# Optimization experiments

Measured on AMD Instinct MI355X. Metric: run time of the kernel, lower is better.

The kernel has to match this reference:

```python
import jax, jax.numpy as jnp
import numpy as np

N_NODES = 1_000_000
N_EDGES = 16_000_000
BATCH = 1_000_000
EMBED_DIM = 3


def setup_inputs() -> dict:
    key = jax.random.key(0)
    ks = jax.random.split(key, 11)
    edge_index = jax.random.randint(ks[0], (2, N_EDGES), 0, N_NODES, dtype=jnp.int32)
    edge_weight = jax.random.uniform(ks[1], (N_EDGES,), dtype=jnp.float32) + 0.1
    home = jax.random.randint(ks[2], (BATCH,), 0, N_NODES, dtype=jnp.int32)
    away = jax.random.randint(ks[3], (BATCH,), 0, N_NODES, dtype=jnp.int32)
    emb = jax.random.normal(ks[4], (N_NODES, EMBED_DIM), dtype=jnp.float32)
    w_conv = jax.random.normal(ks[5], (3, 3), dtype=jnp.float32) * 0.5
    b_conv = jax.random.normal(ks[6], (3,), dtype=jnp.float32) * 0.1
    w1 = jax.random.normal(ks[7], (6, 6), dtype=jnp.float32) * 0.4
    b1 = jax.random.normal(ks[8], (6,), dtype=jnp.float32) * 0.1
    w3 = jax.random.normal(ks[9], (6, 3), dtype=jnp.float32) * 0.4
    b3 = jax.random.normal(ks[10], (3,), dtype=jnp.float32) * 0.1
    return {"edge_index": edge_index, "edge_weight": edge_weight, "home": home,
            "away": away, "emb": emb, "w_conv": w_conv, "b_conv": b_conv,
            "w1": w1, "b1": b1, "w3": w3, "b3": b3}


def reference(edge_index, edge_weight, home, away, emb, w_conv, b_conv, w1, b1, w3, b3):
    n = emb.shape[0]
    row, col = edge_index[0], edge_index[1]
    # gcn_norm (symmetric, add_self_loops=False): deg over target nodes
    deg = jax.ops.segment_sum(edge_weight, col, num_segments=n)
    dinv = jnp.where(deg > 0, jax.lax.rsqrt(jnp.where(deg > 0, deg, 1.0)), 0.0)
    norm = dinv[row] * edge_weight * dinv[col]  # [E]
    x = emb @ w_conv                            # [N,3] transformed features
    msg = norm[:, None] * x[row]                # [E,3] gather + scale
    agg = jax.ops.segment_sum(msg, col, num_segments=n) + b_conv  # [N,3]
    x = jax.nn.leaky_relu(agg)                  # conv1 output
    h = jnp.concatenate([x[home], x[away]], axis=-1)  # [B,6]
    h = jax.nn.leaky_relu(h @ w1 + b1)          # lin1
    h = jax.nn.leaky_relu(h @ w3 + b3)          # lin3 -> [B,3]
    return jax.nn.log_softmax(h, axis=0)        # LogSoftmax over dim=0 as in source
```

## Files before the change

### kernel.cpp

```cpp
#include <hip/hip_runtime.h>
#include <hip/hip_fp16.h>
#include <math.h>

#define NN 1000000
#define NE 16000000
#define NB 1000000
#define NEQ (NE / 4)
#define BN 4096
#define NBUCK 245
#define NBUCKR 256
#define NBLK 1024
#define SSPLIT 4
#define CMASK 0xFFFFFu

__device__ __forceinline__ float leaky(float v) { return v > 0.f ? v : 0.01f * v; }

__device__ __forceinline__ uint2 pack_h4(float x, float y, float z) {
    __half2 a = __floats2half2_rn(x, y);
    __half2 b = __floats2half2_rn(z, 0.f);
    uint2 u;
    u.x = *(unsigned int*)&a;
    u.y = *(unsigned int*)&b;
    return u;
}

__device__ __forceinline__ float3 unpack_h4(uint2 u) {
    __half2 a = *(__half2*)&u.x;
    __half2 b = *(__half2*)&u.y;
    float2 fa = __half22float2(a);
    return make_float3(fa.x, fa.y, __low2float(b));
}

__device__ __forceinline__ void atomicMaxF(float* addr, float val) {
    unsigned int* ia = (unsigned int*)addr;
    unsigned int old = *ia;
    while (true) {
        float f = __uint_as_float(old);
        if (f >= val) break;
        unsigned int prev = atomicCAS(ia, old, __float_as_uint(val));
        if (prev == old) break;
        old = prev;
    }
}

__global__ void init_stats(float* stats) {
    int t = threadIdx.x;
    if (t < 3) stats[t] = -1e30f;
    else if (t < 6) stats[t] = 0.f;
}

__global__ __launch_bounds__(256) void count_kernel(const int4* __restrict__ col4,
                                                    unsigned int* __restrict__ HG) {
    __shared__ unsigned int h[NBUCKR];
    h[threadIdx.x] = 0u;
    __syncthreads();
    int stride = gridDim.x * 256;
    for (int i = blockIdx.x * 256 + threadIdx.x; i < NEQ; i += stride) {
        int4 c = col4[i];
        atomicAdd(&h[((unsigned int)c.x) >> 12], 1u);
        atomicAdd(&h[((unsigned int)c.y) >> 12], 1u);
        atomicAdd(&h[((unsigned int)c.z) >> 12], 1u);
        atomicAdd(&h[((unsigned int)c.w) >> 12], 1u);
    }
    __syncthreads();
    HG[(size_t)threadIdx.x * NBLK + blockIdx.x] = h[threadIdx.x];
}

__global__ __launch_bounds__(256) void scan_sum(const unsigned int* __restrict__ HG,
                                                unsigned int* __restrict__ part) {
    const unsigned int* p = HG + (size_t)blockIdx.x * NBLK;
    unsigned int s = 0;
    for (int i = threadIdx.x; i < NBLK; i += 256) s += p[i];
    #pragma unroll
    for (int off = 32; off > 0; off >>= 1) s += __shfl_down(s, off);
    __shared__ unsigned int sm[4];
    int wave = threadIdx.x >> 6, lane = threadIdx.x & 63;
    if (lane == 0) sm[wave] = s;
    __syncthreads();
    if (threadIdx.x == 0) part[blockIdx.x] = sm[0] + sm[1] + sm[2] + sm[3];
}

__global__ void scan_part(unsigned int* part) {
    __shared__ unsigned int tmp[256];
    int t = threadIdx.x;
    unsigned int v = part[t];
    tmp[t] = v;
    __syncthreads();
    for (int off = 1; off < 256; off <<= 1) {
        unsigned int add = (t >= off) ? tmp[t - off] : 0u;
        __syncthreads();
        tmp[t] += add;
        __syncthreads();
    }
    part[t] = tmp[t] - v;
}

__global__ __launch_bounds__(256) void scan_apply(unsigned int* __restrict__ HG,
                                                  const unsigned int* __restrict__ part) {
    __shared__ unsigned int vals[NBLK];
    __shared__ unsigned int ts[256];
    int t = threadIdx.x;
    unsigned int* p = HG + (size_t)blockIdx.x * NBLK;
    for (int i = t; i < NBLK; i += 256) vals[i] = p[i];
    __syncthreads();
    unsigned int a0 = vals[4 * t], a1 = vals[4 * t + 1], a2 = vals[4 * t + 2], a3 = vals[4 * t + 3];
    unsigned int ls = a0 + a1 + a2 + a3;
    ts[t] = ls;
    __syncthreads();
    for (int off = 1; off < 256; off <<= 1) {
        unsigned int add = (t >= off) ? ts[t - off] : 0u;
        __syncthreads();
        ts[t] += add;
        __syncthreads();
    }
    unsigned int base = part[blockIdx.x] + ts[t] - ls;
    p[4 * t] = base;
    p[4 * t + 1] = base + a0;
    p[4 * t + 2] = base + a0 + a1;
    p[4 * t + 3] = base + a0 + a1 + a2;
}

__global__ __launch_bounds__(256) void scatter_kernel(const int4* __restrict__ row4,
                                                      const int4* __restrict__ col4,
                                                      const float4* __restrict__ w4,
                                                      const unsigned int* __restrict__ HG,
                                                      uint2* __restrict__ rec) {
    __shared__ unsigned int pos[NBUCKR];
    pos[threadIdx.x] = HG[(size_t)threadIdx.x * NBLK + blockIdx.x];
    __syncthreads();
    int stride = gridDim.x * 256;
    for (int i = blockIdx.x * 256 + threadIdx.x; i < NEQ; i += stride) {
        int4 r = row4[i];
        int4 c = col4[i];
        float4 w = w4[i];
        {
            unsigned int cu = (unsigned int)c.x;
            unsigned int p = atomicAdd(&pos[cu >> 12], 1u);
            rec[p] = make_uint2((unsigned int)r.x | ((cu & 4095u) << 20), __float_as_uint(w.x));
        }
        {
            unsigned int cu = (unsigned int)c.y;
            unsigned int p = atomicAdd(&pos[cu >> 12], 1u);
            rec[p] = make_uint2((unsigned int)r.y | ((cu & 4095u) << 20), __float_as_uint(w.y));
        }
        {
            unsigned int cu = (unsigned int)c.z;
            unsigned int p = atomicAdd(&pos[cu >> 12], 1u);
            rec[p] = make_uint2((unsigned int)r.z | ((cu & 4095u) << 20), __float_as_uint(w.z));
        }
        {
            unsigned int cu = (unsigned int)c.w;
            unsigned int p = atomicAdd(&pos[cu >> 12], 1u);
            rec[p] = make_uint2((unsigned int)r.w | ((cu & 4095u) << 20), __float_as_uint(w.w));
        }
    }
}

__global__ __launch_bounds__(512) void bucket_deg_kernel(const uint2* __restrict__ rec,
                                                         const unsigned int* __restrict__ HG,
                                                         float* __restrict__ deg_g) {
    __shared__ float degl[BN];
    int b = blockIdx.x % NBUCK;
    int sp = blockIdx.x / NBUCK;
    for (int t = threadIdx.x; t < BN; t += 512) degl[t] = 0.f;
    unsigned int s0 = HG[(size_t)b * NBLK];
    unsigned int e0 = HG[(size_t)(b + 1) * NBLK];
    unsigned int n = e0 - s0;
    unsigned int beg = s0 + (unsigned int)((unsigned long long)n * sp / SSPLIT);
    unsigned int end = s0 + (unsigned int)((unsigned long long)n * (sp + 1) / SSPLIT);
    __syncthreads();
    unsigned int i = beg + threadIdx.x;
    for (; i + 1536 < end; i += 2048) {
        uint2 r0 = rec[i], r1 = rec[i + 512], r2 = rec[i + 1024], r3 = rec[i + 1536];
        atomicAdd(&degl[r0.x >> 20], __uint_as_float(r0.y));
        atomicAdd(&degl[r1.x >> 20], __uint_as_float(r1.y));
        atomicAdd(&degl[r2.x >> 20], __uint_as_float(r2.y));
        atomicAdd(&degl[r3.x >> 20], __uint_as_float(r3.y));
    }
    for (; i < end; i += 512) {
        uint2 r0 = rec[i];
        atomicAdd(&degl[r0.x >> 20], __uint_as_float(r0.y));
    }
    __syncthreads();
    int node0 = b * BN;
    for (int t = threadIdx.x; t < BN; t += 512) {
        float v = degl[t];
        if (v != 0.f) atomicAdd(&deg_g[node0 + t], v);
    }
}

__global__ __launch_bounds__(256) void node1_kernel(const float* __restrict__ deg_g,
                                                    const float* __restrict__ emb,
                                                    const float* __restrict__ w_conv,
                                                    float* __restrict__ dinv,
                                                    uint2* __restrict__ y) {
    int g = blockIdx.x * 256 + threadIdx.x;
    if (g >= NN) return;
    float d = deg_g[g];
    float di = d > 0.f ? rsqrtf(d) : 0.f;
    dinv[g] = di;
    float e0 = emb[3 * g], e1 = emb[3 * g + 1], e2 = emb[3 * g + 2];
    float x0 = e0 * w_conv[0] + e1 * w_conv[3] + e2 * w_conv[6];
    float x1 = e0 * w_conv[1] + e1 * w_conv[4] + e2 * w_conv[7];
    float x2 = e0 * w_conv[2] + e1 * w_conv[5] + e2 * w_conv[8];
    y[g] = pack_h4(di * x0, di * x1, di * x2);
}

__global__ __launch_bounds__(512) void bucket_agg_kernel(const uint2* __restrict__ rec,
                                                         const unsigned int* __restrict__ HG,
                                                         const uint2* __restrict__ y,
                                                         float* __restrict__ acc_g) {
    __shared__ float acc[BN * 3];
    int b = blockIdx.x % NBUCK;
    int sp = blockIdx.x / NBUCK;
    for (int t = threadIdx.x; t < BN * 3; t += 512) acc[t] = 0.f;
    unsigned int s0 = HG[(size_t)b * NBLK];
    unsigned int e0 = HG[(size_t)(b + 1) * NBLK];
    unsigned int n = e0 - s0;
    unsigned int beg = s0 + (unsigned int)((unsigned long long)n * sp / SSPLIT);
    unsigned int end = s0 + (unsigned int)((unsigned long long)n * (sp + 1) / SSPLIT);
    __syncthreads();
    unsigned int i = beg + threadIdx.x;
    for (; i + 1536 < end; i += 2048) {
        uint2 r0 = rec[i], r1 = rec[i + 512], r2 = rec[i + 1024], r3 = rec[i + 1536];
        uint2 u0 = y[r0.x & CMASK];
        uint2 u1 = y[r1.x & CMASK];
        uint2 u2 = y[r2.x & CMASK];
        uint2 u3 = y[r3.x & CMASK];
        float3 y0 = unpack_h4(u0), y1 = unpack_h4(u1), y2 = unpack_h4(u2), y3 = unpack_h4(u3);
        float w0 = __uint_as_float(r0.y), w1 = __uint_as_float(r1.y);
        float w2 = __uint_as_float(r2.y), w3 = __uint_as_float(r3.y);
        unsigned int c0 = (r0.x >> 20) * 3, c1 = (r1.x >> 20) * 3;
        unsigned int c2 = (r2.x >> 20) * 3, c3 = (r3.x >> 20) * 3;
        atomicAdd(&acc[c0 + 0], w0 * y0.x); atomicAdd(&acc[c0 + 1], w0 * y0.y); atomicAdd(&acc[c0 + 2], w0 * y0.z);
        atomicAdd(&acc[c1 + 0], w1 * y1.x); atomicAdd(&acc[c1 + 1], w1 * y1.y); atomicAdd(&acc[c1 + 2], w1 * y1.z);
        atomicAdd(&acc[c2 + 0], w2 * y2.x); atomicAdd(&acc[c2 + 1], w2 * y2.y); atomicAdd(&acc[c2 + 2], w2 * y2.z);
        atomicAdd(&acc[c3 + 0], w3 * y3.x); atomicAdd(&acc[c3 + 1], w3 * y3.y); atomicAdd(&acc[c3 + 2], w3 * y3.z);
    }
    for (; i < end; i += 512) {
        uint2 r0 = rec[i];
        float3 y0 = unpack_h4(y[r0.x & CMASK]);
        float w0 = __uint_as_float(r0.y);
        unsigned int c0 = (r0.x >> 20) * 3;
        atomicAdd(&acc[c0 + 0], w0 * y0.x); atomicAdd(&acc[c0 + 1], w0 * y0.y); atomicAdd(&acc[c0 + 2], w0 * y0.z);
    }
    __syncthreads();
    size_t base = (size_t)b * BN * 3;
    for (int t = threadIdx.x; t < BN * 3; t += 512) {
        float v = acc[t];
        if (v != 0.f) atomicAdd(&acc_g[base + t], v);
    }
}

__global__ __launch_bounds__(256) void node2_kernel(const float* __restrict__ acc_g,
                                                    const float* __restrict__ dinv,
                                                    const float* __restrict__ b_conv,
                                                    uint2* __restrict__ xf) {
    int g = blockIdx.x * 256 + threadIdx.x;
    if (g >= NN) return;
    float di = dinv[g];
    float a0 = acc_g[3 * (size_t)g], a1 = acc_g[3 * (size_t)g + 1], a2 = acc_g[3 * (size_t)g + 2];
    xf[g] = pack_h4(leaky(di * a0 + b_conv[0]),
                    leaky(di * a1 + b_conv[1]),
                    leaky(di * a2 + b_conv[2]));
}

__global__ __launch_bounds__(256) void batch_kernel(const int4* __restrict__ home4,
                                                    const int4* __restrict__ away4,
                                                    const uint2* __restrict__ xf,
                                                    const float* __restrict__ w1,
                                                    const float* __restrict__ b1,
                                                    const float* __restrict__ w3,
                                                    const float* __restrict__ b3,
                                                    float4* __restrict__ out4,
                                                    float* __restrict__ stats, int nq) {
    int i = blockIdx.x * blockDim.x + threadIdx.x;
    float m0 = -1e30f, m1 = -1e30f, m2 = -1e30f;
    if (i < nq) {
        float W1[36], B1[6], W3[18], B3[3];
        #pragma unroll
        for (int k = 0; k < 36; k++) W1[k] = w1[k];
        #pragma unroll
        for (int k = 0; k < 6; k++) B1[k] = b1[k];
        #pragma unroll
        for (int k = 0; k < 18; k++) W3[k] = w3[k];
        #pragma unroll
        for (int k = 0; k < 3; k++) B3[k] = b3[k];

        int4 hh = home4[i], aa = away4[i];
        int hs[4] = {hh.x, hh.y, hh.z, hh.w};
        int as_[4] = {aa.x, aa.y, aa.z, aa.w};
        float o[12];
        #pragma unroll
        for (int e = 0; e < 4; e++) {
            float3 xh = unpack_h4(xf[hs[e]]);
            float3 xa = unpack_h4(xf[as_[e]]);
            float h[6] = {xh.x, xh.y, xh.z, xa.x, xa.y, xa.z};
            float l1v[6];
            #pragma unroll
            for (int j = 0; j < 6; j++) {
                float s = B1[j];
                #pragma unroll
                for (int k = 0; k < 6; k++) s += h[k] * W1[k * 6 + j];
                l1v[j] = leaky(s);
            }
            float o3[3];
            #pragma unroll
            for (int j = 0; j < 3; j++) {
                float s = B3[j];
                #pragma unroll
                for (int k = 0; k < 6; k++) s += l1v[k] * W3[k * 3 + j];
                o3[j] = leaky(s);
            }
            o[3 * e + 0] = o3[0];
            o[3 * e + 1] = o3[1];
            o[3 * e + 2] = o3[2];
            m0 = fmaxf(m0, o3[0]);
            m1 = fmaxf(m1, o3[1]);
            m2 = fmaxf(m2, o3[2]);
        }
        #pragma unroll
        for (int q = 0; q < 3; q++)
            out4[3 * (size_t)i + q] = make_float4(o[4 * q], o[4 * q + 1], o[4 * q + 2], o[4 * q + 3]);
    }
    #pragma unroll
    for (int off = 32; off > 0; off >>= 1) {
        m0 = fmaxf(m0, __shfl_down(m0, off));
        m1 = fmaxf(m1, __shfl_down(m1, off));
        m2 = fmaxf(m2, __shfl_down(m2, off));
    }
    __shared__ float sm[3][4];
    int wave = threadIdx.x >> 6, lane = threadIdx.x & 63;
    if (lane == 0) { sm[0][wave] = m0; sm[1][wave] = m1; sm[2][wave] = m2; }
    __syncthreads();
    if (threadIdx.x == 0) {
        atomicMaxF(&stats[0], fmaxf(fmaxf(sm[0][0], sm[0][1]), fmaxf(sm[0][2], sm[0][3])));
        atomicMaxF(&stats[1], fmaxf(fmaxf(sm[1][0], sm[1][1]), fmaxf(sm[1][2], sm[1][3])));
        atomicMaxF(&stats[2], fmaxf(fmaxf(sm[2][0], sm[2][1]), fmaxf(sm[2][2], sm[2][3])));
    }
}

__global__ __launch_bounds__(256) void sumexp_kernel(const float4* __restrict__ out4,
                                                     float* __restrict__ stats, int nq) {
    float mx0 = stats[0], mx1 = stats[1], mx2 = stats[2];
    int i = blockIdx.x * blockDim.x + threadIdx.x;
    float s0 = 0.f, s1 = 0.f, s2 = 0.f;
    if (i < nq) {
        float4 v = out4[i];
        float vals[4] = {v.x, v.y, v.z, v.w};
        int c = (4 * i) % 3;
        #pragma unroll
        for (int e = 0; e < 4; e++) {
            float mv = (c == 0) ? mx0 : ((c == 1) ? mx1 : mx2);
            float ee = expf(vals[e] - mv);
            if (c == 0) s0 += ee; else if (c == 1) s1 += ee; else s2 += ee;
            c = (c == 2) ? 0 : (c + 1);
        }
    }
    #pragma unroll
    for (int off = 32; off > 0; off >>= 1) {
        s0 += __shfl_down(s0, off);
        s1 += __shfl_down(s1, off);
        s2 += __shfl_down(s2, off);
    }
    __shared__ float sm[3][4];
    int wave = threadIdx.x >> 6, lane = threadIdx.x & 63;
    if (lane == 0) { sm[0][wave] = s0; sm[1][wave] = s1; sm[2][wave] = s2; }
    __syncthreads();
    if (threadIdx.x == 0) {
        atomicAdd(&stats[3], sm[0][0] + sm[0][1] + sm[0][2] + sm[0][3]);
        atomicAdd(&stats[4], sm[1][0] + sm[1][1] + sm[1][2] + sm[1][3]);
        atomicAdd(&stats[5], sm[2][0] + sm[2][1] + sm[2][2] + sm[2][3]);
    }
}

__global__ __launch_bounds__(256) void final_kernel(float4* __restrict__ out4,
                                                    const float* __restrict__ stats, int nq) {
    float o0 = stats[0] + logf(stats[3]);
    float o1 = stats[1] + logf(stats[4]);
    float o2 = stats[2] + logf(stats[5]);
    int i = blockIdx.x * blockDim.x + threadIdx.x;
    if (i >= nq) return;
    float4 v = out4[i];
    float vals[4] = {v.x, v.y, v.z, v.w};
    int c = (4 * i) % 3;
    #pragma unroll
    for (int e = 0; e < 4; e++) {
        vals[e] -= (c == 0) ? o0 : ((c == 1) ? o1 : o2);
        c = (c == 2) ? 0 : (c + 1);
    }
    out4[i] = make_float4(vals[0], vals[1], vals[2], vals[3]);
}

extern "C" void kernel_launch(void* const* d_in, const int* in_sizes, int n_in,
                              void* d_out, int out_size, void* d_ws, size_t ws_size,
                              hipStream_t stream) {
    const int*   edge_index  = (const int*)d_in[0];
    const float* edge_weight = (const float*)d_in[1];
    const int*   home        = (const int*)d_in[2];
    const int*   away        = (const int*)d_in[3];
    const float* emb         = (const float*)d_in[4];
    const float* w_conv      = (const float*)d_in[5];
    const float* b_conv      = (const float*)d_in[6];
    const float* w1          = (const float*)d_in[7];
    const float* b1          = (const float*)d_in[8];
    const float* w3          = (const float*)d_in[9];
    const float* b3          = (const float*)d_in[10];
    float* out = (float*)d_out;

    char* ws = (char*)d_ws;
    uint2*        rec   = (uint2*)(ws);
    unsigned int* HG    = (unsigned int*)(ws + 128000000);
    unsigned int* part  = (unsigned int*)(ws + 129048576);
    float*        deg_g = (float*)(ws + 129049600);
    float*        dinv  = (float*)(ws + 133063680);
    uint2*        y     = (uint2*)(ws + 137063680);
    float*        acc_g = (float*)(ws + 145063680);
    uint2*        xf    = (uint2*)(ws + 157105920);
    float*        stats = (float*)(ws + 165105920);

    const int* row = edge_index;
    const int* col = edge_index + NE;

    init_stats<<<1, 64, 0, stream>>>(stats);
    hipMemsetAsync(deg_g, 0, 4014080, stream);
    hipMemsetAsync(acc_g, 0, 12042240, stream);

    count_kernel<<<NBLK, 256, 0, stream>>>((const int4*)col, HG);
    scan_sum<<<NBUCKR, 256, 0, stream>>>(HG, part);
    scan_part<<<1, 256, 0, stream>>>(part);
    scan_apply<<<NBUCKR, 256, 0, stream>>>(HG, part);
    scatter_kernel<<<NBLK, 256, 0, stream>>>((const int4*)row, (const int4*)col,
                                             (const float4*)edge_weight, HG, rec);

    bucket_deg_kernel<<<NBUCK * SSPLIT, 512, 0, stream>>>(rec, HG, deg_g);
    node1_kernel<<<(NN + 255) / 256, 256, 0, stream>>>(deg_g, emb, w_conv, dinv, y);
    bucket_agg_kernel<<<NBUCK * SSPLIT, 512, 0, stream>>>(rec, HG, y, acc_g);
    node2_kernel<<<(NN + 255) / 256, 256, 0, stream>>>(acc_g, dinv, b_conv, xf);

    const int BQ = NB / 4;
    const int OQ = (NB * 3) / 4;
    batch_kernel<<<(BQ + 255) / 256, 256, 0, stream>>>((const int4*)home, (const int4*)away, xf,
                                                       w1, b1, w3, b3, (float4*)out, stats, BQ);
    sumexp_kernel<<<(OQ + 255) / 256, 256, 0, stream>>>((const float4*)out, stats, OQ);
    final_kernel<<<(OQ + 255) / 256, 256, 0, stream>>>((float4*)out, stats, OQ);
}
```

Measured before the change: 929.0 us.

## Pack node features into 32-bit shared-exponent format and use nontemporal streaming loads

Replaces the 8-byte fp16x4 node feature encoding with a custom 32-bit format (three 9-bit signed mantissas sharing a 5-bit exponent), halving the bytes of random gathers in the aggregation and batch kernels. It also switches streaming reads of edges, records and indices to nontemporal loads and deepens the bucket loops to eight records per iteration so more gathers are in flight. The cost is lower precision of the intermediate features (about 8 bits per component relative to the largest of the three), which could hurt accuracy against the reference.

```diff
diff --git a/kernel.cpp b/kernel.cpp
--- a/kernel.cpp
+++ b/kernel.cpp
@@ -1,5 +1,4 @@
 #include <hip/hip_runtime.h>
-#include <hip/hip_fp16.h>
 #include <math.h>
 
 #define NN 1000000
@@ -13,22 +12,30 @@
 #define SSPLIT 4
 #define CMASK 0xFFFFFu
 
+typedef int   i32x4 __attribute__((ext_vector_type(4)));
+typedef float f32x4 __attribute__((ext_vector_type(4)));
+
 __device__ __forceinline__ float leaky(float v) { return v > 0.f ? v : 0.01f * v; }
 
-__device__ __forceinline__ uint2 pack_h4(float x, float y, float z) {
-    __half2 a = __floats2half2_rn(x, y);
-    __half2 b = __floats2half2_rn(z, 0.f);
-    uint2 u;
-    u.x = *(unsigned int*)&a;
-    u.y = *(unsigned int*)&b;
-    return u;
-}
-
-__device__ __forceinline__ float3 unpack_h4(uint2 u) {
-    __half2 a = *(__half2*)&u.x;
-    __half2 b = *(__half2*)&u.y;
-    float2 fa = __half22float2(a);
-    return make_float3(fa.x, fa.y, __low2float(b));
+__device__ __forceinline__ unsigned int pack_bf32(float x, float y, float z) {
+    float m = fmaxf(fmaxf(fabsf(x), fabsf(y)), fabsf(z));
+    int ex = ((int)(__float_as_uint(m) >> 23) & 0xFF) - 126;
+    ex = min(max(ex, -20), 11);
+    float scale = __uint_as_float((unsigned int)(135 - ex) << 23);
+    int qx = min(max(__float2int_rn(x * scale), -255), 255);
+    int qy = min(max(__float2int_rn(y * scale), -255), 255);
+    int qz = min(max(__float2int_rn(z * scale), -255), 255);
+    return ((unsigned int)(qx & 0x1FF)) | ((unsigned int)(qy & 0x1FF) << 9) |
+           ((unsigned int)(qz & 0x1FF) << 18) | ((unsigned int)(ex + 20) << 27);
+}
+
+__device__ __forceinline__ float3 unpack_bf32(unsigned int u) {
+    int qx = ((int)(u << 23)) >> 23;
+    int qy = ((int)(u << 14)) >> 23;
+    int qz = ((int)(u << 5)) >> 23;
+    int ex = (int)(u >> 27) - 20;
+    float s = __uint_as_float((unsigned int)(ex + 119) << 23);
+    return make_float3(qx * s, qy * s, qz * s);
 }
 
 __device__ __forceinline__ void atomicMaxF(float* addr, float val) {
@@ -49,14 +56,14 @@
     else if (t < 6) stats[t] = 0.f;
 }
 
-__global__ __launch_bounds__(256) void count_kernel(const int4* __restrict__ col4,
+__global__ __launch_bounds__(256) void count_kernel(const i32x4* __restrict__ col4,
                                                     unsigned int* __restrict__ HG) {
     __shared__ unsigned int h[NBUCKR];
     h[threadIdx.x] = 0u;
     __syncthreads();
     int stride = gridDim.x * 256;
     for (int i = blockIdx.x * 256 + threadIdx.x; i < NEQ; i += stride) {
-        int4 c = col4[i];
+        i32x4 c = __builtin_nontemporal_load(col4 + i);
         atomicAdd(&h[((unsigned int)c.x) >> 12], 1u);
         atomicAdd(&h[((unsigned int)c.y) >> 12], 1u);
         atomicAdd(&h[((unsigned int)c.z) >> 12], 1u);
@@ -120,9 +127,9 @@
     p[4 * t + 3] = base + a0 + a1 + a2;
 }
 
-__global__ __launch_bounds__(256) void scatter_kernel(const int4* __restrict__ row4,
-                                                      const int4* __restrict__ col4,
-                                                      const float4* __restrict__ w4,
+__global__ __launch_bounds__(256) void scatter_kernel(const i32x4* __restrict__ row4,
+                                                      const i32x4* __restrict__ col4,
+                                                      const f32x4* __restrict__ w4,
                                                       const unsigned int* __restrict__ HG,
                                                       uint2* __restrict__ rec) {
     __shared__ unsigned int pos[NBUCKR];
@@ -130,9 +137,9 @@
     __syncthreads();
     int stride = gridDim.x * 256;
     for (int i = blockIdx.x * 256 + threadIdx.x; i < NEQ; i += stride) {
-        int4 r = row4[i];
-        int4 c = col4[i];
-        float4 w = w4[i];
+        i32x4 r = __builtin_nontemporal_load(row4 + i);
+        i32x4 c = __builtin_nontemporal_load(col4 + i);
+        f32x4 w = __builtin_nontemporal_load(w4 + i);
         {
             unsigned int cu = (unsigned int)c.x;
             unsigned int p = atomicAdd(&pos[cu >> 12], 1u);
@@ -156,7 +163,7 @@
     }
 }
 
-__global__ __launch_bounds__(512) void bucket_deg_kernel(const uint2* __restrict__ rec,
+__global__ __launch_bounds__(512) void bucket_deg_kernel(const unsigned long long* __restrict__ rec,
                                                          const unsigned int* __restrict__ HG,
                                                          float* __restrict__ deg_g) {
     __shared__ float degl[BN];
@@ -170,16 +177,17 @@
     unsigned int end = s0 + (unsigned int)((unsigned long long)n * (sp + 1) / SSPLIT);
     __syncthreads();
     unsigned int i = beg + threadIdx.x;
-    for (; i + 1536 < end; i += 2048) {
-        uint2 r0 = rec[i], r1 = rec[i + 512], r2 = rec[i + 1024], r3 = rec[i + 1536];
-        atomicAdd(&degl[r0.x >> 20], __uint_as_float(r0.y));
-        atomicAdd(&degl[r1.x >> 20], __uint_as_float(r1.y));
-        atomicAdd(&degl[r2.x >> 20], __uint_as_float(r2.y));
-        atomicAdd(&degl[r3.x >> 20], __uint_as_float(r3.y));
+    for (; i + 3584 < end; i += 4096) {
+        unsigned long long r[8];
+        #pragma unroll
+        for (int k = 0; k < 8; k++) r[k] = __builtin_nontemporal_load(rec + i + k * 512);
+        #pragma unroll
+        for (int k = 0; k < 8; k++)
+            atomicAdd(&degl[((unsigned int)r[k]) >> 20], __uint_as_float((unsigned int)(r[k] >> 32)));
     }
     for (; i < end; i += 512) {
-        uint2 r0 = rec[i];
-        atomicAdd(&degl[r0.x >> 20], __uint_as_float(r0.y));
+        unsigned long long r0 = __builtin_nontemporal_load(rec + i);
+        atomicAdd(&degl[((unsigned int)r0) >> 20], __uint_as_float((unsigned int)(r0 >> 32)));
     }
     __syncthreads();
     int node0 = b * BN;
@@ -193,7 +201,7 @@
                                                     const float* __restrict__ emb,
                                                     const float* __restrict__ w_conv,
                                                     float* __restrict__ dinv,
-                                                    uint2* __restrict__ y) {
+                                                    unsigned int* __restrict__ y) {
     int g = blockIdx.x * 256 + threadIdx.x;
     if (g >= NN) return;
     float d = deg_g[g];
@@ -203,12 +211,12 @@
     float x0 = e0 * w_conv[0] + e1 * w_conv[3] + e2 * w_conv[6];
     float x1 = e0 * w_conv[1] + e1 * w_conv[4] + e2 * w_conv[7];
     float x2 = e0 * w_conv[2] + e1 * w_conv[5] + e2 * w_conv[8];
-    y[g] = pack_h4(di * x0, di * x1, di * x2);
-}
-
-__global__ __launch_bounds__(512) void bucket_agg_kernel(const uint2* __restrict__ rec,
+    y[g] = pack_bf32(di * x0, di * x1, di * x2);
+}
+
+__global__ __launch_bounds__(512) void bucket_agg_kernel(const unsigned long long* __restrict__ rec,
                                                          const unsigned int* __restrict__ HG,
-                                                         const uint2* __restrict__ y,
+                                                         const unsigned int* __restrict__ y,
                                                          float* __restrict__ acc_g) {
     __shared__ float acc[BN * 3];
     int b = blockIdx.x % NBUCK;
@@ -221,28 +229,31 @@
     unsigned int end = s0 + (unsigned int)((unsigned long long)n * (sp + 1) / SSPLIT);
     __syncthreads();
     unsigned int i = beg + threadIdx.x;
-    for (; i + 1536 < end; i += 2048) {
-        uint2 r0 = rec[i], r1 = rec[i + 512], r2 = rec[i + 1024], r3 = rec[i + 1536];
-        uint2 u0 = y[r0.x & CMASK];
-        uint2 u1 = y[r1.x & CMASK];
-        uint2 u2 = y[r2.x & CMASK];
-        uint2 u3 = y[r3.x & CMASK];
-        float3 y0 = unpack_h4(u0), y1 = unpack_h4(u1), y2 = unpack_h4(u2), y3 = unpack_h4(u3);
-        float w0 = __uint_as_float(r0.y), w1 = __uint_as_float(r1.y);
-        float w2 = __uint_as_float(r2.y), w3 = __uint_as_float(r3.y);
-        unsigned int c0 = (r0.x >> 20) * 3, c1 = (r1.x >> 20) * 3;
-        unsigned int c2 = (r2.x >> 20) * 3, c3 = (r3.x >> 20) * 3;
-        atomicAdd(&acc[c0 + 0], w0 * y0.x); atomicAdd(&acc[c0 + 1], w0 * y0.y); atomicAdd(&acc[c0 + 2], w0 * y0.z);
-        atomicAdd(&acc[c1 + 0], w1 * y1.x); atomicAdd(&acc[c1 + 1], w1 * y1.y); atomicAdd(&acc[c1 + 2], w1 * y1.z);
-        atomicAdd(&acc[c2 + 0], w2 * y2.x); atomicAdd(&acc[c2 + 1], w2 * y2.y); atomicAdd(&acc[c2 + 2], w2 * y2.z);
-        atomicAdd(&acc[c3 + 0], w3 * y3.x); atomicAdd(&acc[c3 + 1], w3 * y3.y); atomicAdd(&acc[c3 + 2], w3 * y3.z);
+    for (; i + 3584 < end; i += 4096) {
+        unsigned long long r[8];
+        #pragma unroll
+        for (int k = 0; k < 8; k++) r[k] = __builtin_nontemporal_load(rec + i + k * 512);
+        unsigned int yu[8];
+        #pragma unroll
+        for (int k = 0; k < 8; k++) yu[k] = y[((unsigned int)r[k]) & CMASK];
+        #pragma unroll
+        for (int k = 0; k < 8; k++) {
+            float w = __uint_as_float((unsigned int)(r[k] >> 32));
+            float3 yv = unpack_bf32(yu[k]);
+            unsigned int c = (((unsigned int)r[k]) >> 20) * 3;
+            atomicAdd(&acc[c + 0], w * yv.x);
+            atomicAdd(&acc[c + 1], w * yv.y);
+            atomicAdd(&acc[c + 2], w * yv.z);
+        }
     }
     for (; i < end; i += 512) {
-        uint2 r0 = rec[i];
-        float3 y0 = unpack_h4(y[r0.x & CMASK]);
-        float w0 = __uint_as_float(r0.y);
-        unsigned int c0 = (r0.x >> 20) * 3;
-        atomicAdd(&acc[c0 + 0], w0 * y0.x); atomicAdd(&acc[c0 + 1], w0 * y0.y); atomicAdd(&acc[c0 + 2], w0 * y0.z);
+        unsigned long long r0 = __builtin_nontemporal_load(rec + i);
+        float w = __uint_as_float((unsigned int)(r0 >> 32));
+        float3 yv = unpack_bf32(y[((unsigned int)r0) & CMASK]);
+        unsigned int c = (((unsigned int)r0) >> 20) * 3;
+        atomicAdd(&acc[c + 0], w * yv.x);
+        atomicAdd(&acc[c + 1], w * yv.y);
+        atomicAdd(&acc[c + 2], w * yv.z);
     }
     __syncthreads();
     size_t base = (size_t)b * BN * 3;
@@ -255,19 +266,19 @@
 __global__ __launch_bounds__(256) void node2_kernel(const float* __restrict__ acc_g,
                                                     const float* __restrict__ dinv,
                                                     const float* __restrict__ b_conv,
-                                                    uint2* __restrict__ xf) {
+                                                    unsigned int* __restrict__ xf) {
     int g = blockIdx.x * 256 + threadIdx.x;
     if (g >= NN) return;
     float di = dinv[g];
     float a0 = acc_g[3 * (size_t)g], a1 = acc_g[3 * (size_t)g + 1], a2 = acc_g[3 * (size_t)g + 2];
-    xf[g] = pack_h4(leaky(di * a0 + b_conv[0]),
-                    leaky(di * a1 + b_conv[1]),
-                    leaky(di * a2 + b_conv[2]));
-}
-
-__global__ __launch_bounds__(256) void batch_kernel(const int4* __restrict__ home4,
-                                                    const int4* __restrict__ away4,
-                                                    const uint2* __restrict__ xf,
+    xf[g] = pack_bf32(leaky(di * a0 + b_conv[0]),
+                      leaky(di * a1 + b_conv[1]),
+                      leaky(di * a2 + b_conv[2]));
+}
+
+__global__ __launch_bounds__(256) void batch_kernel(const i32x4* __restrict__ home4,
+                                                    const i32x4* __restrict__ away4,
+                                                    const unsigned int* __restrict__ xf,
                                                     const float* __restrict__ w1,
                                                     const float* __restrict__ b1,
                                                     const float* __restrict__ w3,
@@ -287,14 +298,15 @@
         #pragma unroll
         for (int k = 0; k < 3; k++) B3[k] = b3[k];
 
-        int4 hh = home4[i], aa = away4[i];
+        i32x4 hh = __builtin_nontemporal_load(home4 + i);
+        i32x4 aa = __builtin_nontemporal_load(away4 + i);
         int hs[4] = {hh.x, hh.y, hh.z, hh.w};
         int as_[4] = {aa.x, aa.y, aa.z, aa.w};
         float o[12];
         #pragma unroll
         for (int e = 0; e < 4; e++) {
-            float3 xh = unpack_h4(xf[hs[e]]);
-            float3 xa = unpack_h4(xf[as_[e]]);
+            float3 xh = unpack_bf32(xf[hs[e]]);
+            float3 xa = unpack_bf32(xf[as_[e]]);
             float h[6] = {xh.x, xh.y, xh.z, xa.x, xa.y, xa.z};
             float l1v[6];
             #pragma unroll
@@ -414,10 +426,10 @@
     unsigned int* part  = (unsigned int*)(ws + 129048576);
     float*        deg_g = (float*)(ws + 129049600);
     float*        dinv  = (float*)(ws + 133063680);
-    uint2*        y     = (uint2*)(ws + 137063680);
-    float*        acc_g = (float*)(ws + 145063680);
-    uint2*        xf    = (uint2*)(ws + 157105920);
-    float*        stats = (float*)(ws + 165105920);
+    unsigned int* y     = (unsigned int*)(ws + 137063680);
+    float*        acc_g = (float*)(ws + 141063680);
+    unsigned int* xf    = (unsigned int*)(ws + 153105920);
+    float*        stats = (float*)(ws + 157105920);
 
     const int* row = edge_index;
     const int* col = edge_index + NE;
@@ -426,21 +438,21 @@
     hipMemsetAsync(deg_g, 0, 4014080, stream);
     hipMemsetAsync(acc_g, 0, 12042240, stream);
 
-    count_kernel<<<NBLK, 256, 0, stream>>>((const int4*)col, HG);
+    count_kernel<<<NBLK, 256, 0, stream>>>((const i32x4*)col, HG);
     scan_sum<<<NBUCKR, 256, 0, stream>>>(HG, part);
     scan_part<<<1, 256, 0, stream>>>(part);
     scan_apply<<<NBUCKR, 256, 0, stream>>>(HG, part);
-    scatter_kernel<<<NBLK, 256, 0, stream>>>((const int4*)row, (const int4*)col,
-                                             (const float4*)edge_weight, HG, rec);
-
-    bucket_deg_kernel<<<NBUCK * SSPLIT, 512, 0, stream>>>(rec, HG, deg_g);
+    scatter_kernel<<<NBLK, 256, 0, stream>>>((const i32x4*)row, (const i32x4*)col,
+                                             (const f32x4*)edge_weight, HG, rec);
+
+    bucket_deg_kernel<<<NBUCK * SSPLIT, 512, 0, stream>>>((const unsigned long long*)rec, HG, deg_g);
     node1_kernel<<<(NN + 255) / 256, 256, 0, stream>>>(deg_g, emb, w_conv, dinv, y);
-    bucket_agg_kernel<<<NBUCK * SSPLIT, 512, 0, stream>>>(rec, HG, y, acc_g);
+    bucket_agg_kernel<<<NBUCK * SSPLIT, 512, 0, stream>>>((const unsigned long long*)rec, HG, y, acc_g);
     node2_kernel<<<(NN + 255) / 256, 256, 0, stream>>>(acc_g, dinv, b_conv, xf);
 
     const int BQ = NB / 4;
     const int OQ = (NB * 3) / 4;
-    batch_kernel<<<(BQ + 255) / 256, 256, 0, stream>>>((const int4*)home, (const int4*)away, xf,
+    batch_kernel<<<(BQ + 255) / 256, 256, 0, stream>>>((const i32x4*)home, (const i32x4*)away, xf,
                                                        w1, b1, w3, b3, (float4*)out, stats, BQ);
     sumexp_kernel<<<(OQ + 255) / 256, 256, 0, stream>>>((const float4*)out, stats, OQ);
     final_kernel<<<(OQ + 255) / 256, 256, 0, stream>>>((float4*)out, stats, OQ);
```

New measurement: 918.2 us. Within noise of the previous version (-1.2%).
